# Optimization experiments

Hardware: AMD Instinct MI355X
Metric: run time of the kernel (lower is better)

Reference implementation:

```python
import jax, jax.numpy as jnp
import numpy as np
from jax import lax

N, D, M, H = 8192, 32, 8, 128
ATOL = 1e-5
RTOL = 1e-5
MAX_STEPS = 10   # bounded adaptive dopri5 iterations (accept/reject with masking)
DT0 = 0.25


def setup_inputs() -> dict:
    key = jax.random.key(0)
    ks = jax.random.split(key, 6)
    p = lambda k, shape, s: jax.random.normal(k, shape, jnp.float32) * s
    return {
        "z": jax.random.normal(ks[0], (N, D), jnp.float32),
        "G_w": p(ks[1], (M, D), 0.3),
        "W1": p(ks[2], (H, D), (1.0 / D) ** 0.5),
        "b1": jnp.zeros((H,), jnp.float32),
        "W2": p(ks[3], (H, H), (1.0 / H) ** 0.5),
        "b2": jnp.zeros((H,), jnp.float32),
        "W3": p(ks[4], (D, H), (1.0 / H) ** 0.5),
        "b3": jnp.zeros((D,), jnp.float32),
        "T": jnp.ones((1,), jnp.float32),
    }


def qpnf_forward(z, G_w, W1, b1, W2, b2, W3, b3, T):
    d = z.shape[1]

    def mlp(x):  # dF network: d -> 128 -> 128 -> d
        h = jax.nn.relu(x @ W1.T + b1)
        h = jax.nn.relu(h @ W2.T + b2)
        return h @ W3.T + b3

    # G is linear (no bias) so jacrev(G)(x) == G_w for every sample; the batched
    # dG @ dG^T solves collapse to one shared (m,m) solve / (d,d) projector.
    A = G_w @ G_w.T                       # (m, m)
    AinvG = jnp.linalg.solve(A, G_w)      # (m, d) = A^{-1} W
    P = G_w.T @ AinvG                     # (d, d) null-space projector W^T A^{-1} W
    IP = jnp.eye(d, dtype=z.dtype) - P
    trP = jnp.trace(P)

    jac_mlp = jax.vmap(jax.jacrev(lambda xi: mlp(xi[None, :])[0]))  # (N,d,d)

    def f(y):  # augmented state y = [x | logp], dlogp/dt = -div(dx/dx)
        x = y[:, :d]
        dF = mlp(x)                        # (N, d)
        g = x @ G_w.T                      # (N, m)
        dz = -(dF @ IP) - g @ AinvG        # -(eta_J) - (eta_C)
        JdF = jac_mlp(x)                   # (N, d, d)
        # J_f = -(I-P) JdF - P  ->  dlogp = -trace(J_f)
        dlogp = jnp.einsum('jk,nkj->n', IP, JdF) + trP
        return jnp.concatenate([dz, dlogp[:, None]], axis=1)

    def rk_step(y, dt):  # Dormand-Prince 5(4)
        k1 = f(y)
        k2 = f(y + dt * (0.2 * k1))
        k3 = f(y + dt * (3/40 * k1 + 9/40 * k2))
        k4 = f(y + dt * (44/45 * k1 - 56/15 * k2 + 32/9 * k3))
        k5 = f(y + dt * (19372/6561 * k1 - 25360/2187 * k2 + 64448/6561 * k3 - 212/729 * k4))
        k6 = f(y + dt * (9017/3168 * k1 - 355/33 * k2 + 46732/5247 * k3 + 49/176 * k4 - 5103/18656 * k5))
        y1 = y + dt * (35/384 * k1 + 500/1113 * k3 + 125/192 * k4 - 2187/6784 * k5 + 11/84 * k6)
        k7 = f(y1)
        err = dt * ((35/384 - 5179/57600) * k1 + (500/1113 - 7571/16695) * k3
                    + (125/192 - 393/640) * k4 + (-2187/6784 + 92097/339200) * k5
                    + (11/84 - 187/2100) * k6 - (1/40) * k7)
        return y1, err

    t1 = 2.0 * T[0]  # eval path: integration_times[-1] *= 2
    y0 = jnp.concatenate([z, jnp.zeros((z.shape[0], 1), z.dtype)], axis=1)

    def body(carry, _):
        t, dt, y = carry
        done = t >= t1 - 1e-9
        dtc = jnp.where(done, jnp.asarray(1e-3, z.dtype), jnp.minimum(dt, t1 - t))
        y1, ev = rk_step(y, dtc)
        tol = ATOL + RTOL * jnp.maximum(jnp.abs(y), jnp.abs(y1))
        errn = jnp.sqrt(jnp.mean((ev / tol) ** 2))
        accept = jnp.logical_and(~done, errn <= 1.0)
        y_new = jnp.where(accept, y1, y)
        t_new = jnp.where(accept, t + dtc, t)
        factor = jnp.clip(0.9 * errn ** (-0.2), 0.2, 10.0)
        dt_new = jnp.where(done, dt, jnp.clip(dtc * factor, 1e-6, t1))
        dt_new = lax.stop_gradient(dt_new)
        return (t_new, dt_new, y_new), None

    init = (jnp.asarray(0.0, z.dtype), jnp.asarray(DT0, z.dtype), y0)
    (_, _, yT), _ = lax.scan(body, init, None, length=MAX_STEPS)
    return yT[:, :d]


def reference(z, G_w, W1, b1, W2, b2, W3, b3, T):
    return qpnf_forward(z, G_w, W1, b1, W2, b2, W3, b3, T)
```

## Files before the change

### kernel.cpp

```cpp
#include <hip/hip_runtime.h>
#include <hip/hip_cooperative_groups.h>
#include <math.h>

namespace cg = cooperative_groups;
typedef float4 f4;

#define NT 512
#define RB 32

#define WS_R     0
#define WS_W2T   16384
#define WS_PART  32768
#define WS_YZ    35328
#define WS_Y1Z   297472
#define WS_YL    559616
#define WS_Y1L   567808
#define WS_KZ    576000
#define WS_KL    2411008
#define WS_TOTAL 2468352

#define L_W1T   0
#define L_C3    4096
#define L_P     8192
#define L_HST   9216
#define L_XST   13824
#define L_B1    14976
#define L_B2    15104
#define L_C0    15232
#define L_GS    15264
#define L_AAUG  15520
#define L_AINVG 15648
#define L_MISC  15904
#define LDS_FLOATS 15905
#define L_RED   L_XST

__device__ const float ACO[5][5] = {
  { 0.2f, 0.f, 0.f, 0.f, 0.f },
  { (float)(3.0/40.0), (float)(9.0/40.0), 0.f, 0.f, 0.f },
  { (float)(44.0/45.0), (float)(-56.0/15.0), (float)(32.0/9.0), 0.f, 0.f },
  { (float)(19372.0/6561.0), (float)(-25360.0/2187.0), (float)(64448.0/6561.0), (float)(-212.0/729.0), 0.f },
  { (float)(9017.0/3168.0), (float)(-355.0/33.0), (float)(46732.0/5247.0), (float)(49.0/176.0), (float)(-5103.0/18656.0) }
};

#define B1C ((float)(35.0/384.0))
#define B3C ((float)(500.0/1113.0))
#define B4C ((float)(125.0/192.0))
#define B5C ((float)(-2187.0/6784.0))
#define B6C ((float)(11.0/84.0))

#define E1C ((float)(35.0/384.0 - 5179.0/57600.0))
#define E3C ((float)(500.0/1113.0 - 7571.0/16695.0))
#define E4C ((float)(125.0/192.0 - 393.0/640.0))
#define E5C ((float)(-2187.0/6784.0 + 92097.0/339200.0))
#define E6C ((float)(11.0/84.0 - 187.0/2100.0))
#define E7C ((float)(-1.0/40.0))

__device__ __forceinline__ f4 ld4(const float* p){ return *(const f4*)p; }
__device__ __forceinline__ void st4(float* p, f4 v){ *(f4*)p = v; }

__device__ void assemble_x(float* lds, const float* __restrict__ ws, int r0, int tid,
                           float dtc, const float* co, int np)
{
  __syncthreads();
  if (tid < 256){
    const int r = tid >> 3, jj = (tid & 7) * 4;
    const int base = (r0 + r) * 32 + jj;
    f4 y = ld4(&ws[WS_YZ + base]);
    float sx = 0.f, sy = 0.f, sz = 0.f, sw = 0.f;
    for (int p = 0; p < np; p++){
      f4 kv = ld4(&ws[WS_KZ + p * 262144 + base]);
      float c = co[p];
      sx += c * kv.x; sy += c * kv.y; sz += c * kv.z; sw += c * kv.w;
    }
    lds[L_XST + (jj + 0) * 36 + r] = y.x + dtc * sx;
    lds[L_XST + (jj + 1) * 36 + r] = y.y + dtc * sy;
    lds[L_XST + (jj + 2) * 36 + r] = y.z + dtc * sz;
    lds[L_XST + (jj + 3) * 36 + r] = y.w + dtc * sw;
  }
  __syncthreads();
}

__device__ void eval_f(float* lds, float* __restrict__ ws, int r0, int tid,
                       float trP, int kout)
{
  const int cg = tid & 31, kh = (tid >> 5) & 1, wv = tid >> 6;
  const int row4 = 4 * wv;

  float a1[4][4];
#pragma unroll
  for (int i = 0; i < 4; i++)
#pragma unroll
    for (int j = 0; j < 4; j++) a1[i][j] = 0.f;
#pragma unroll 4
  for (int t = 0; t < 16; t++){
    const int k = kh * 16 + t;
    f4 av = ld4(&lds[L_XST + k * 36 + row4]);
    f4 bv = ld4(&lds[L_W1T + k * 128 + 4 * cg]);
    const float* ap = (const float*)&av;
    const float* bp = (const float*)&bv;
#pragma unroll
    for (int i = 0; i < 4; i++)
#pragma unroll
      for (int j = 0; j < 4; j++) a1[i][j] += bp[i] * ap[j];
  }
#pragma unroll
  for (int i = 0; i < 4; i++)
#pragma unroll
    for (int j = 0; j < 4; j++) a1[i][j] += __shfl_xor(a1[i][j], 32);
  if (kh == 0){
    f4 b1v = ld4(&lds[L_B1 + 4 * cg]);
    const float* b1p = (const float*)&b1v;
#pragma unroll
    for (int i = 0; i < 4; i++){
      f4 hv; float* hp = (float*)&hv;
#pragma unroll
      for (int j = 0; j < 4; j++) hp[j] = fmaxf(a1[i][j] + b1p[i], 0.f);
      st4(&lds[L_HST + (4 * cg + i) * 36 + row4], hv);
    }
  }
  __syncthreads();

  float ah[4][4], at[4][4];
#pragma unroll
  for (int i = 0; i < 4; i++)
#pragma unroll
    for (int j = 0; j < 4; j++){ ah[i][j] = 0.f; at[i][j] = 0.f; }
  const f4* W2T4 = (const f4*)&ws[WS_W2T];
  const f4* R4   = (const f4*)&ws[WS_R];
  const int kb = kh * 64;
  f4 wb[4], rb[4];
#pragma unroll
  for (int u = 0; u < 4; u++){
    wb[u] = W2T4[(kb + u) * 32 + cg];
    rb[u] = R4[(kb + u) * 32 + cg];
  }
#pragma unroll 1
  for (int g = 0; g < 16; g++){
    f4 wc[4], rc[4];
#pragma unroll
    for (int u = 0; u < 4; u++){ wc[u] = wb[u]; rc[u] = rb[u]; }
    if (g < 15){
      const int kn = kb + (g + 1) * 4;
#pragma unroll
      for (int u = 0; u < 4; u++){
        wb[u] = W2T4[(kn + u) * 32 + cg];
        rb[u] = R4[(kn + u) * 32 + cg];
      }
    }
#pragma unroll
    for (int u = 0; u < 4; u++){
      const int k = kb + g * 4 + u;
      f4 av = ld4(&lds[L_HST + k * 36 + row4]);
      const float* ap = (const float*)&av;
      const float* wp = (const float*)&wc[u];
      const float* rp = (const float*)&rc[u];
      float m[4];
#pragma unroll
      for (int j = 0; j < 4; j++) m[j] = (ap[j] > 0.f) ? 1.f : 0.f;
#pragma unroll
      for (int i = 0; i < 4; i++)
#pragma unroll
        for (int j = 0; j < 4; j++){
          ah[i][j] += wp[i] * ap[j];
          at[i][j] += rp[i] * m[j];
        }
    }
  }
#pragma unroll
  for (int i = 0; i < 4; i++)
#pragma unroll
    for (int j = 0; j < 4; j++){
      ah[i][j] += __shfl_xor(ah[i][j], 32);
      at[i][j] += __shfl_xor(at[i][j], 32);
    }

  f4 b2v = ld4(&lds[L_B2 + 4 * cg]);
  const float* b2p = (const float*)&b2v;
  float h2v[4][4]; float dl[4] = {0.f, 0.f, 0.f, 0.f};
#pragma unroll
  for (int i = 0; i < 4; i++)
#pragma unroll
    for (int j = 0; j < 4; j++){
      float pre = ah[i][j] + b2p[i];
      float hv = fmaxf(pre, 0.f);
      h2v[i][j] = hv;
      if (pre > 0.f) dl[j] += at[i][j];
    }
#pragma unroll
  for (int mk = 1; mk < 32; mk <<= 1){
#pragma unroll
    for (int j = 0; j < 4; j++) dl[j] += __shfl_xor(dl[j], mk, 64);
  }
  __syncthreads();
  if (kh == 0){
#pragma unroll
    for (int i = 0; i < 4; i++){
      f4 hv; float* hp = (float*)&hv;
#pragma unroll
      for (int j = 0; j < 4; j++) hp[j] = h2v[i][j];
      st4(&lds[L_HST + (4 * cg + i) * 36 + row4], hv);
    }
    if (cg == 0){
#pragma unroll
      for (int j = 0; j < 4; j++)
        ws[WS_KL + kout * 8192 + r0 + row4 + j] = dl[j] + trP;
    }
  }
  __syncthreads();

  float a3[4] = {0.f, 0.f, 0.f, 0.f};
#pragma unroll 8
  for (int t = 0; t < 64; t++){
    const int b = kh * 64 + t;
    f4 av = ld4(&lds[L_HST + b * 36 + row4]);
    const float* ap = (const float*)&av;
    float w3 = lds[L_C3 + b * 32 + cg];
#pragma unroll
    for (int j = 0; j < 4; j++) a3[j] += ap[j] * w3;
  }
#pragma unroll 8
  for (int t = 0; t < 16; t++){
    const int q = kh * 16 + t;
    f4 av = ld4(&lds[L_XST + q * 36 + row4]);
    const float* ap = (const float*)&av;
    float pv = lds[L_P + q * 32 + cg];
#pragma unroll
    for (int j = 0; j < 4; j++) a3[j] += ap[j] * pv;
  }
#pragma unroll
  for (int j = 0; j < 4; j++) a3[j] += __shfl_xor(a3[j], 32);
  if (kh == 0){
    float c0v = lds[L_C0 + cg];
#pragma unroll
    for (int j = 0; j < 4; j++)
      ws[WS_KZ + kout * 262144 + (r0 + row4 + j) * 32 + cg] = -(a3[j] + c0v);
  }
}

__global__ void __launch_bounds__(NT, 2)
qpnf_kernel(const float* __restrict__ z, const float* __restrict__ Gw,
            const float* __restrict__ W1g, const float* __restrict__ b1g,
            const float* __restrict__ W2g, const float* __restrict__ b2g,
            const float* __restrict__ W3g, const float* __restrict__ b3g,
            const float* __restrict__ Tg, float* __restrict__ out,
            float* __restrict__ ws)
{
  __shared__ float lds[LDS_FLOATS];
  const int tid = threadIdx.x;
  const int bid = blockIdx.x;
  const int r0 = bid * RB;
  cg::grid_group grid = cg::this_grid();

  for (int i = 0; i < 8; i++){
    int idx = tid + i * NT;
    int h = idx >> 5, j = idx & 31;
    lds[L_W1T + j * 128 + h] = W1g[idx];
  }
  if (tid < 128){ lds[L_B1 + tid] = b1g[tid]; lds[L_B2 + tid] = b2g[tid]; }
  if (tid < 256) lds[L_GS + tid] = Gw[tid];
  __syncthreads();

  if (tid < 64){
    int i = tid >> 3, j = tid & 7;
    float s = 0.f;
    for (int k = 0; k < 32; k++) s += lds[L_GS + i * 32 + k] * lds[L_GS + j * 32 + k];
    lds[L_AAUG + i * 16 + j] = s;
    lds[L_AAUG + i * 16 + 8 + j] = (i == j) ? 1.f : 0.f;
  }
  __syncthreads();
  if (tid == 0){
    float* A = &lds[L_AAUG];
    for (int c = 0; c < 8; c++){
      int p = c; float mx = fabsf(A[c * 16 + c]);
      for (int r = c + 1; r < 8; r++){
        float v = fabsf(A[r * 16 + c]);
        if (v > mx){ mx = v; p = r; }
      }
      if (p != c)
        for (int q = 0; q < 16; q++){ float t = A[c*16+q]; A[c*16+q] = A[p*16+q]; A[p*16+q] = t; }
      float pv = 1.0f / A[c * 16 + c];
      for (int q = 0; q < 16; q++) A[c * 16 + q] *= pv;
      for (int r = 0; r < 8; r++) if (r != c){
        float fct = A[r * 16 + c];
        for (int q = 0; q < 16; q++) A[r * 16 + q] -= fct * A[c * 16 + q];
      }
    }
  }
  __syncthreads();
  if (tid < 256){
    int m = tid >> 5, d = tid & 31;
    float s = 0.f;
    for (int q = 0; q < 8; q++) s += lds[L_AAUG + m * 16 + 8 + q] * lds[L_GS + q * 32 + d];
    lds[L_AINVG + m * 32 + d] = s;
  }
  __syncthreads();
  for (int i4 = 0; i4 < 2; i4++){
    int idx = tid + i4 * NT;
    int i = idx >> 5, j = idx & 31;
    float s = 0.f;
    for (int m = 0; m < 8; m++) s += lds[L_GS + m * 32 + i] * lds[L_AINVG + m * 32 + j];
    lds[L_P + i * 32 + j] = s;
  }
  __syncthreads();
  float* IPl = &lds[L_XST];
  for (int i4 = 0; i4 < 2; i4++){
    int idx = tid + i4 * NT;
    int i = idx >> 5, j = idx & 31;
    IPl[i * 32 + j] = ((i == j) ? 1.f : 0.f) - lds[L_P + i * 32 + j];
  }
  if (tid == 0){
    float s = 0.f;
    for (int i = 0; i < 32; i++) s += lds[L_P + i * 32 + i];
    lds[L_MISC] = s;
  }
  __syncthreads();
  for (int i4 = 0; i4 < 8; i4++){
    int idx = tid + i4 * NT;
    int b = idx >> 5, c = idx & 31;
    float s = 0.f;
    for (int i = 0; i < 32; i++) s += W3g[i * 128 + b] * IPl[i * 32 + c];
    lds[L_C3 + b * 32 + c] = s;
  }
  if (tid < 32){
    float s = 0.f;
    for (int i = 0; i < 32; i++) s += b3g[i] * IPl[i * 32 + tid];
    lds[L_C0 + tid] = s;
  }
  for (int i4 = 0; i4 < 8; i4++){
    int idx = tid + i4 * NT;
    int j = idx >> 7, b = idx & 127;
    float s = 0.f;
    for (int k = 0; k < 32; k++) s += IPl[j * 32 + k] * W3g[k * 128 + b];
    lds[L_HST + j * 128 + b] = s;
  }
  __syncthreads();
  if (bid < 128 && tid < 128){
    int a = bid;
    float s = 0.f;
    for (int j = 0; j < 32; j++) s += W1g[a * 32 + j] * lds[L_HST + j * 128 + tid];
    ws[WS_R + a * 128 + tid] = s * W2g[tid * 128 + a];
  }
  if (bid >= 128 && tid < 128){
    int a = bid - 128;
    ws[WS_W2T + a * 128 + tid] = W2g[tid * 128 + a];
  }
  if (tid < 256){
    const int r = tid >> 3, jj = (tid & 7) * 4;
    const int base = (r0 + r) * 32 + jj;
    st4(&ws[WS_YZ + base], ld4(&z[base]));
  }
  if (tid < RB) ws[WS_YL + r0 + tid] = 0.f;

  const float trP = lds[L_MISC];
  const float t1 = 2.0f * Tg[0];

  grid.sync();

  float t_cur = 0.f, dt_cur = 0.25f;
  bool prev_acc = false;

  for (int step = 0; step < 10; step++){
    if (t_cur >= t1 - 1e-9f) break;
    const float dtc = fminf(dt_cur, t1 - t_cur);

    for (int s = 1; s <= 6; s++){
      if (s == 1 && step > 0){
        if (prev_acc){
          if (tid < 256){
            const int r = tid >> 3, jj = (tid & 7) * 4;
            const int base = (r0 + r) * 32 + jj;
            st4(&ws[WS_KZ + 0 * 262144 + base], ld4(&ws[WS_KZ + 6 * 262144 + base]));
          }
          if (tid < RB) ws[WS_KL + 0 * 8192 + r0 + tid] = ws[WS_KL + 6 * 8192 + r0 + tid];
        }
        continue;
      }
      assemble_x(lds, ws, r0, tid, dtc, ACO[s >= 2 ? s - 2 : 0], s - 1);
      eval_f(lds, ws, r0, tid, trP, s - 1);
    }

    __syncthreads();
    if (tid < 256){
      const int r = tid >> 3, jj = (tid & 7) * 4;
      const int base = (r0 + r) * 32 + jj;
      f4 y   = ld4(&ws[WS_YZ + base]);
      f4 k1v = ld4(&ws[WS_KZ + 0 * 262144 + base]);
      f4 k3v = ld4(&ws[WS_KZ + 2 * 262144 + base]);
      f4 k4v = ld4(&ws[WS_KZ + 3 * 262144 + base]);
      f4 k5v = ld4(&ws[WS_KZ + 4 * 262144 + base]);
      f4 k6v = ld4(&ws[WS_KZ + 5 * 262144 + base]);
      f4 x;
      x.x = y.x + dtc * (B1C*k1v.x + B3C*k3v.x + B4C*k4v.x + B5C*k5v.x + B6C*k6v.x);
      x.y = y.y + dtc * (B1C*k1v.y + B3C*k3v.y + B4C*k4v.y + B5C*k5v.y + B6C*k6v.y);
      x.z = y.z + dtc * (B1C*k1v.z + B3C*k3v.z + B4C*k4v.z + B5C*k5v.z + B6C*k6v.z);
      x.w = y.w + dtc * (B1C*k1v.w + B3C*k3v.w + B4C*k4v.w + B5C*k5v.w + B6C*k6v.w);
      st4(&ws[WS_Y1Z + base], x);
      lds[L_XST + (jj + 0) * 36 + r] = x.x;
      lds[L_XST + (jj + 1) * 36 + r] = x.y;
      lds[L_XST + (jj + 2) * 36 + r] = x.z;
      lds[L_XST + (jj + 3) * 36 + r] = x.w;
    }
    if (tid < RB){
      int n = r0 + tid;
      float s = B1C * ws[WS_KL + 0*8192 + n] + B3C * ws[WS_KL + 2*8192 + n]
              + B4C * ws[WS_KL + 3*8192 + n] + B5C * ws[WS_KL + 4*8192 + n]
              + B6C * ws[WS_KL + 5*8192 + n];
      ws[WS_Y1L + n] = ws[WS_YL + n] + dtc * s;
    }
    __syncthreads();
    eval_f(lds, ws, r0, tid, trP, 6);
    __syncthreads();

    float sacc = 0.f;
    if (tid < 256){
      const int r = tid >> 3, jj = (tid & 7) * 4;
      const int base = (r0 + r) * 32 + jj;
      f4 k1v = ld4(&ws[WS_KZ + 0 * 262144 + base]);
      f4 k3v = ld4(&ws[WS_KZ + 2 * 262144 + base]);
      f4 k4v = ld4(&ws[WS_KZ + 3 * 262144 + base]);
      f4 k5v = ld4(&ws[WS_KZ + 4 * 262144 + base]);
      f4 k6v = ld4(&ws[WS_KZ + 5 * 262144 + base]);
      f4 k7v = ld4(&ws[WS_KZ + 6 * 262144 + base]);
      f4 yv  = ld4(&ws[WS_YZ + base]);
      f4 y1v = ld4(&ws[WS_Y1Z + base]);
      float ev, tol, q;
      ev = dtc * (E1C*k1v.x + E3C*k3v.x + E4C*k4v.x + E5C*k5v.x + E6C*k6v.x + E7C*k7v.x);
      tol = 1e-5f + 1e-5f * fmaxf(fabsf(yv.x), fabsf(y1v.x)); q = ev / tol; sacc += q * q;
      ev = dtc * (E1C*k1v.y + E3C*k3v.y + E4C*k4v.y + E5C*k5v.y + E6C*k6v.y + E7C*k7v.y);
      tol = 1e-5f + 1e-5f * fmaxf(fabsf(yv.y), fabsf(y1v.y)); q = ev / tol; sacc += q * q;
      ev = dtc * (E1C*k1v.z + E3C*k3v.z + E4C*k4v.z + E5C*k5v.z + E6C*k6v.z + E7C*k7v.z);
      tol = 1e-5f + 1e-5f * fmaxf(fabsf(yv.z), fabsf(y1v.z)); q = ev / tol; sacc += q * q;
      ev = dtc * (E1C*k1v.w + E3C*k3v.w + E4C*k4v.w + E5C*k5v.w + E6C*k6v.w + E7C*k7v.w);
      tol = 1e-5f + 1e-5f * fmaxf(fabsf(yv.w), fabsf(y1v.w)); q = ev / tol; sacc += q * q;
    }
    if (tid < RB){
      int n = r0 + tid;
      float evl = dtc * (E1C * ws[WS_KL + 0*8192 + n] + E3C * ws[WS_KL + 2*8192 + n]
                + E4C * ws[WS_KL + 3*8192 + n] + E5C * ws[WS_KL + 4*8192 + n]
                + E6C * ws[WS_KL + 5*8192 + n] + E7C * ws[WS_KL + 6*8192 + n]);
      float toll = 1e-5f + 1e-5f * fmaxf(fabsf(ws[WS_YL + n]), fabsf(ws[WS_Y1L + n]));
      float ql = evl / toll; sacc += ql * ql;
    }
    lds[L_RED + tid] = sacc; __syncthreads();
    for (int o = 256; o > 0; o >>= 1){
      if (tid < o) lds[L_RED + tid] += lds[L_RED + tid + o];
      __syncthreads();
    }
    if (tid == 0) ws[WS_PART + step * 256 + bid] = lds[L_RED + 0];

    grid.sync();

    if (tid < 256) lds[L_RED + tid] = ws[WS_PART + step * 256 + tid];
    __syncthreads();
    for (int o = 128; o > 0; o >>= 1){
      if (tid < o) lds[L_RED + tid] += lds[L_RED + tid + o];
      __syncthreads();
    }
    const float errn = sqrtf(lds[L_RED + 0] / 270336.0f);
    __syncthreads();

    const bool accept = (errn <= 1.0f);
    if (accept){
      if (tid < 256){
        const int r = tid >> 3, jj = (tid & 7) * 4;
        const int base = (r0 + r) * 32 + jj;
        st4(&ws[WS_YZ + base], ld4(&ws[WS_Y1Z + base]));
      }
      if (tid < RB) ws[WS_YL + r0 + tid] = ws[WS_Y1L + r0 + tid];
      t_cur += dtc;
    }
    float fac = 0.9f * powf(errn, -0.2f);
    fac = fminf(fmaxf(fac, 0.2f), 10.0f);
    dt_cur = fminf(fmaxf(dtc * fac, 1e-6f), t1);
    prev_acc = accept;
  }

  if (tid < 256){
    const int r = tid >> 3, jj = (tid & 7) * 4;
    const int base = (r0 + r) * 32 + jj;
    st4(&out[base], ld4(&ws[WS_YZ + base]));
  }
}

extern "C" void kernel_launch(void* const* d_in, const int* in_sizes, int n_in,
                              void* d_out, int out_size, void* d_ws, size_t ws_size,
                              hipStream_t stream)
{
  (void)in_sizes; (void)n_in; (void)out_size;
  const float* z  = (const float*)d_in[0];
  const float* Gw = (const float*)d_in[1];
  const float* W1 = (const float*)d_in[2];
  const float* b1 = (const float*)d_in[3];
  const float* W2 = (const float*)d_in[4];
  const float* b2 = (const float*)d_in[5];
  const float* W3 = (const float*)d_in[6];
  const float* b3 = (const float*)d_in[7];
  const float* T  = (const float*)d_in[8];
  float* out = (float*)d_out;
  float* ws  = (float*)d_ws;
  if (ws_size < (size_t)WS_TOTAL * sizeof(float)) return;

  void* args[] = { (void*)&z, (void*)&Gw, (void*)&W1, (void*)&b1, (void*)&W2,
                   (void*)&b2, (void*)&W3, (void*)&b3, (void*)&T, (void*)&out,
                   (void*)&ws };
  hipLaunchCooperativeKernel((const void*)qpnf_kernel, dim3(256), dim3(NT),
                             args, 0, stream);
}
```

Baseline: 1.336 ms.

## Split layer-2 matmul and Jacobian-trace work across two 512-thread groups

The block doubles from 512 to 1024 threads. One half computes the W2 forward product and the output layer, and the other half computes the R-weighted ReLU-mask product used for the divergence term. This halves the per-thread register accumulators and doubles the waves available to hide latency. The cost is idle threads in the layer-1 stage, extra LDS traffic because the mask is re-read from shared memory, and a larger block that may limit occupancy or the cooperative-launch residency. The L_RED reduction buffer must now hold 1024 entries, and it is unclear whether it was sized for that.

Result: slower. 1.644 ms (+23.1%).

```diff
diff --git a/kernel.cpp b/kernel.cpp
--- a/kernel.cpp
+++ b/kernel.cpp
@@ -5,7 +5,7 @@
 namespace cg = cooperative_groups;
 typedef float4 f4;
 
-#define NT 512
+#define NT 1024
 #define RB 32
 
 #define WS_R     0
@@ -83,161 +83,185 @@
 __device__ void eval_f(float* lds, float* __restrict__ ws, int r0, int tid,
                        float trP, int kout)
 {
-  const int cg = tid & 31, kh = (tid >> 5) & 1, wv = tid >> 6;
+  const int cg = tid & 31, kh = (tid >> 5) & 1, wv = (tid >> 6) & 7, grp = tid >> 9;
   const int row4 = 4 * wv;
 
-  float a1[4][4];
+  if (grp == 0){
+    float a1[4][4];
+#pragma unroll
+    for (int i = 0; i < 4; i++)
+#pragma unroll
+      for (int j = 0; j < 4; j++) a1[i][j] = 0.f;
+#pragma unroll 4
+    for (int t = 0; t < 16; t++){
+      const int k = kh * 16 + t;
+      f4 av = ld4(&lds[L_XST + k * 36 + row4]);
+      f4 bv = ld4(&lds[L_W1T + k * 128 + 4 * cg]);
+      const float* ap = (const float*)&av;
+      const float* bp = (const float*)&bv;
+#pragma unroll
+      for (int i = 0; i < 4; i++)
+#pragma unroll
+        for (int j = 0; j < 4; j++) a1[i][j] += bp[i] * ap[j];
+    }
+#pragma unroll
+    for (int i = 0; i < 4; i++)
+#pragma unroll
+      for (int j = 0; j < 4; j++) a1[i][j] += __shfl_xor(a1[i][j], 32);
+    if (kh == 0){
+      f4 b1v = ld4(&lds[L_B1 + 4 * cg]);
+      const float* b1p = (const float*)&b1v;
+#pragma unroll
+      for (int i = 0; i < 4; i++){
+        f4 hv; float* hp = (float*)&hv;
+#pragma unroll
+        for (int j = 0; j < 4; j++) hp[j] = fmaxf(a1[i][j] + b1p[i], 0.f);
+        st4(&lds[L_HST + (4 * cg + i) * 36 + row4], hv);
+      }
+    }
+  }
+  __syncthreads();
+
+  const int kb = kh * 64;
+  float ac[4][4];
 #pragma unroll
   for (int i = 0; i < 4; i++)
 #pragma unroll
-    for (int j = 0; j < 4; j++) a1[i][j] = 0.f;
-#pragma unroll 4
-  for (int t = 0; t < 16; t++){
-    const int k = kh * 16 + t;
-    f4 av = ld4(&lds[L_XST + k * 36 + row4]);
-    f4 bv = ld4(&lds[L_W1T + k * 128 + 4 * cg]);
-    const float* ap = (const float*)&av;
-    const float* bp = (const float*)&bv;
+    for (int j = 0; j < 4; j++) ac[i][j] = 0.f;
+
+  const f4* M4 = (const f4*)&ws[(grp == 0) ? WS_W2T : WS_R];
+  f4 mb[4];
+#pragma unroll
+  for (int u = 0; u < 4; u++) mb[u] = M4[(kb + u) * 32 + cg];
+
+  if (grp == 0){
+#pragma unroll 1
+    for (int g = 0; g < 16; g++){
+      f4 mc[4];
+#pragma unroll
+      for (int u = 0; u < 4; u++) mc[u] = mb[u];
+      if (g < 15){
+        const int kn = kb + (g + 1) * 4;
+#pragma unroll
+        for (int u = 0; u < 4; u++) mb[u] = M4[(kn + u) * 32 + cg];
+      }
+#pragma unroll
+      for (int u = 0; u < 4; u++){
+        const int k = kb + g * 4 + u;
+        f4 av = ld4(&lds[L_HST + k * 36 + row4]);
+        const float* ap = (const float*)&av;
+        const float* wp = (const float*)&mc[u];
+#pragma unroll
+        for (int i = 0; i < 4; i++)
+#pragma unroll
+          for (int j = 0; j < 4; j++) ac[i][j] += wp[i] * ap[j];
+      }
+    }
+  } else {
+#pragma unroll 1
+    for (int g = 0; g < 16; g++){
+      f4 mc[4];
+#pragma unroll
+      for (int u = 0; u < 4; u++) mc[u] = mb[u];
+      if (g < 15){
+        const int kn = kb + (g + 1) * 4;
+#pragma unroll
+        for (int u = 0; u < 4; u++) mb[u] = M4[(kn + u) * 32 + cg];
+      }
+#pragma unroll
+      for (int u = 0; u < 4; u++){
+        const int k = kb + g * 4 + u;
+        f4 av = ld4(&lds[L_HST + k * 36 + row4]);
+        const float* ap = (const float*)&av;
+        const float* rp = (const float*)&mc[u];
+        float m[4];
+#pragma unroll
+        for (int j = 0; j < 4; j++) m[j] = (ap[j] > 0.f) ? 1.f : 0.f;
+#pragma unroll
+        for (int i = 0; i < 4; i++)
+#pragma unroll
+          for (int j = 0; j < 4; j++) ac[i][j] += rp[i] * m[j];
+      }
+    }
+  }
+#pragma unroll
+  for (int i = 0; i < 4; i++)
+#pragma unroll
+    for (int j = 0; j < 4; j++) ac[i][j] += __shfl_xor(ac[i][j], 32);
+
+  float h2v[4][4];
+  if (grp == 0){
+    f4 b2v = ld4(&lds[L_B2 + 4 * cg]);
+    const float* b2p = (const float*)&b2v;
 #pragma unroll
     for (int i = 0; i < 4; i++)
 #pragma unroll
-      for (int j = 0; j < 4; j++) a1[i][j] += bp[i] * ap[j];
-  }
-#pragma unroll
-  for (int i = 0; i < 4; i++)
-#pragma unroll
-    for (int j = 0; j < 4; j++) a1[i][j] += __shfl_xor(a1[i][j], 32);
-  if (kh == 0){
-    f4 b1v = ld4(&lds[L_B1 + 4 * cg]);
-    const float* b1p = (const float*)&b1v;
+      for (int j = 0; j < 4; j++) h2v[i][j] = fmaxf(ac[i][j] + b2p[i], 0.f);
+  }
+  __syncthreads();
+  if (grp == 0 && kh == 0){
 #pragma unroll
     for (int i = 0; i < 4; i++){
       f4 hv; float* hp = (float*)&hv;
 #pragma unroll
-      for (int j = 0; j < 4; j++) hp[j] = fmaxf(a1[i][j] + b1p[i], 0.f);
-      st4(&lds[L_HST + (4 * cg + i) * 36 + row4], hv);
-    }
-  }
-  __syncthreads();
-
-  float ah[4][4], at[4][4];
-#pragma unroll
-  for (int i = 0; i < 4; i++)
-#pragma unroll
-    for (int j = 0; j < 4; j++){ ah[i][j] = 0.f; at[i][j] = 0.f; }
-  const f4* W2T4 = (const f4*)&ws[WS_W2T];
-  const f4* R4   = (const f4*)&ws[WS_R];
-  const int kb = kh * 64;
-  f4 wb[4], rb[4];
-#pragma unroll
-  for (int u = 0; u < 4; u++){
-    wb[u] = W2T4[(kb + u) * 32 + cg];
-    rb[u] = R4[(kb + u) * 32 + cg];
-  }
-#pragma unroll 1
-  for (int g = 0; g < 16; g++){
-    f4 wc[4], rc[4];
-#pragma unroll
-    for (int u = 0; u < 4; u++){ wc[u] = wb[u]; rc[u] = rb[u]; }
-    if (g < 15){
-      const int kn = kb + (g + 1) * 4;
-#pragma unroll
-      for (int u = 0; u < 4; u++){
-        wb[u] = W2T4[(kn + u) * 32 + cg];
-        rb[u] = R4[(kn + u) * 32 + cg];
-      }
-    }
-#pragma unroll
-    for (int u = 0; u < 4; u++){
-      const int k = kb + g * 4 + u;
-      f4 av = ld4(&lds[L_HST + k * 36 + row4]);
-      const float* ap = (const float*)&av;
-      const float* wp = (const float*)&wc[u];
-      const float* rp = (const float*)&rc[u];
-      float m[4];
-#pragma unroll
-      for (int j = 0; j < 4; j++) m[j] = (ap[j] > 0.f) ? 1.f : 0.f;
-#pragma unroll
-      for (int i = 0; i < 4; i++)
-#pragma unroll
-        for (int j = 0; j < 4; j++){
-          ah[i][j] += wp[i] * ap[j];
-          at[i][j] += rp[i] * m[j];
-        }
-    }
-  }
-#pragma unroll
-  for (int i = 0; i < 4; i++)
-#pragma unroll
-    for (int j = 0; j < 4; j++){
-      ah[i][j] += __shfl_xor(ah[i][j], 32);
-      at[i][j] += __shfl_xor(at[i][j], 32);
-    }
-
-  f4 b2v = ld4(&lds[L_B2 + 4 * cg]);
-  const float* b2p = (const float*)&b2v;
-  float h2v[4][4]; float dl[4] = {0.f, 0.f, 0.f, 0.f};
-#pragma unroll
-  for (int i = 0; i < 4; i++)
-#pragma unroll
-    for (int j = 0; j < 4; j++){
-      float pre = ah[i][j] + b2p[i];
-      float hv = fmaxf(pre, 0.f);
-      h2v[i][j] = hv;
-      if (pre > 0.f) dl[j] += at[i][j];
-    }
-#pragma unroll
-  for (int mk = 1; mk < 32; mk <<= 1){
-#pragma unroll
-    for (int j = 0; j < 4; j++) dl[j] += __shfl_xor(dl[j], mk, 64);
-  }
-  __syncthreads();
-  if (kh == 0){
-#pragma unroll
-    for (int i = 0; i < 4; i++){
-      f4 hv; float* hp = (float*)&hv;
-#pragma unroll
       for (int j = 0; j < 4; j++) hp[j] = h2v[i][j];
       st4(&lds[L_HST + (4 * cg + i) * 36 + row4], hv);
     }
-    if (cg == 0){
+  }
+  __syncthreads();
+
+  if (grp == 1){
+    float dl[4] = {0.f, 0.f, 0.f, 0.f};
+#pragma unroll
+    for (int i = 0; i < 4; i++){
+      f4 hv = ld4(&lds[L_HST + (4 * cg + i) * 36 + row4]);
+      const float* hp = (const float*)&hv;
+#pragma unroll
+      for (int j = 0; j < 4; j++)
+        if (hp[j] > 0.f) dl[j] += ac[i][j];
+    }
+#pragma unroll
+    for (int mk = 1; mk < 32; mk <<= 1){
+#pragma unroll
+      for (int j = 0; j < 4; j++) dl[j] += __shfl_xor(dl[j], mk, 64);
+    }
+    if (kh == 0 && cg == 0){
 #pragma unroll
       for (int j = 0; j < 4; j++)
         ws[WS_KL + kout * 8192 + r0 + row4 + j] = dl[j] + trP;
     }
-  }
-  __syncthreads();
-
-  float a3[4] = {0.f, 0.f, 0.f, 0.f};
+  } else {
+    float a3[4] = {0.f, 0.f, 0.f, 0.f};
 #pragma unroll 8
-  for (int t = 0; t < 64; t++){
-    const int b = kh * 64 + t;
-    f4 av = ld4(&lds[L_HST + b * 36 + row4]);
-    const float* ap = (const float*)&av;
-    float w3 = lds[L_C3 + b * 32 + cg];
-#pragma unroll
-    for (int j = 0; j < 4; j++) a3[j] += ap[j] * w3;
-  }
+    for (int t = 0; t < 64; t++){
+      const int b = kh * 64 + t;
+      f4 av = ld4(&lds[L_HST + b * 36 + row4]);
+      const float* ap = (const float*)&av;
+      float w3 = lds[L_C3 + b * 32 + cg];
+#pragma unroll
+      for (int j = 0; j < 4; j++) a3[j] += ap[j] * w3;
+    }
 #pragma unroll 8
-  for (int t = 0; t < 16; t++){
-    const int q = kh * 16 + t;
-    f4 av = ld4(&lds[L_XST + q * 36 + row4]);
-    const float* ap = (const float*)&av;
-    float pv = lds[L_P + q * 32 + cg];
-#pragma unroll
-    for (int j = 0; j < 4; j++) a3[j] += ap[j] * pv;
-  }
-#pragma unroll
-  for (int j = 0; j < 4; j++) a3[j] += __shfl_xor(a3[j], 32);
-  if (kh == 0){
-    float c0v = lds[L_C0 + cg];
-#pragma unroll
-    for (int j = 0; j < 4; j++)
-      ws[WS_KZ + kout * 262144 + (r0 + row4 + j) * 32 + cg] = -(a3[j] + c0v);
+    for (int t = 0; t < 16; t++){
+      const int q = kh * 16 + t;
+      f4 av = ld4(&lds[L_XST + q * 36 + row4]);
+      const float* ap = (const float*)&av;
+      float pv = lds[L_P + q * 32 + cg];
+#pragma unroll
+      for (int j = 0; j < 4; j++) a3[j] += ap[j] * pv;
+    }
+#pragma unroll
+    for (int j = 0; j < 4; j++) a3[j] += __shfl_xor(a3[j], 32);
+    if (kh == 0){
+      float c0v = lds[L_C0 + cg];
+#pragma unroll
+      for (int j = 0; j < 4; j++)
+        ws[WS_KZ + kout * 262144 + (r0 + row4 + j) * 32 + cg] = -(a3[j] + c0v);
+    }
   }
 }
 
-__global__ void __launch_bounds__(NT, 2)
+__global__ void __launch_bounds__(NT, 4)
 qpnf_kernel(const float* __restrict__ z, const float* __restrict__ Gw,
             const float* __restrict__ W1g, const float* __restrict__ b1g,
             const float* __restrict__ W2g, const float* __restrict__ b2g,
@@ -251,7 +275,7 @@
   const int r0 = bid * RB;
   cg::grid_group grid = cg::this_grid();
 
-  for (int i = 0; i < 8; i++){
+  for (int i = 0; i < 4; i++){
     int idx = tid + i * NT;
     int h = idx >> 5, j = idx & 31;
     lds[L_W1T + j * 128 + h] = W1g[idx];
@@ -294,18 +318,16 @@
     lds[L_AINVG + m * 32 + d] = s;
   }
   __syncthreads();
-  for (int i4 = 0; i4 < 2; i4++){
-    int idx = tid + i4 * NT;
-    int i = idx >> 5, j = idx & 31;
+  {
+    int i = tid >> 5, j = tid & 31;
     float s = 0.f;
     for (int m = 0; m < 8; m++) s += lds[L_GS + m * 32 + i] * lds[L_AINVG + m * 32 + j];
     lds[L_P + i * 32 + j] = s;
   }
   __syncthreads();
   float* IPl = &lds[L_XST];
-  for (int i4 = 0; i4 < 2; i4++){
-    int idx = tid + i4 * NT;
-    int i = idx >> 5, j = idx & 31;
+  {
+    int i = tid >> 5, j = tid & 31;
     IPl[i * 32 + j] = ((i == j) ? 1.f : 0.f) - lds[L_P + i * 32 + j];
   }
   if (tid == 0){
@@ -314,7 +336,7 @@
     lds[L_MISC] = s;
   }
   __syncthreads();
-  for (int i4 = 0; i4 < 8; i4++){
+  for (int i4 = 0; i4 < 4; i4++){
     int idx = tid + i4 * NT;
     int b = idx >> 5, c = idx & 31;
     float s = 0.f;
@@ -326,7 +348,7 @@
     for (int i = 0; i < 32; i++) s += b3g[i] * IPl[i * 32 + tid];
     lds[L_C0 + tid] = s;
   }
-  for (int i4 = 0; i4 < 8; i4++){
+  for (int i4 = 0; i4 < 4; i4++){
     int idx = tid + i4 * NT;
     int j = idx >> 7, b = idx & 127;
     float s = 0.f;
@@ -442,7 +464,7 @@
       float ql = evl / toll; sacc += ql * ql;
     }
     lds[L_RED + tid] = sacc; __syncthreads();
-    for (int o = 256; o > 0; o >>= 1){
+    for (int o = 512; o > 0; o >>= 1){
       if (tid < o) lds[L_RED + tid] += lds[L_RED + tid + o];
       __syncthreads();
     }
```

## Interleave W2T/R weights, transpose C3/P in LDS, double-buffer hidden tile

Applied to the files above, without the earlier changes.

Interleaves the W2 transpose and R matrices row by row in one workspace array, so each k-row's two float4 loads fall in the same region. Stores C3 and P transposed in LDS with padded strides, which lets the layer-3 and projector loops read four weights per float4 load instead of one scalar at a time. Writes the second hidden activation into a separate LDS buffer, which removes one __syncthreads between the layer-2 epilogue and the store. The cost is more LDS per block (about 21.8K floats instead of 15.9K), which could reduce occupancy under launch_bounds(512,2).

New measurement: 1.360 ms. About the same (+1.8%).

```diff
diff --git a/kernel.cpp b/kernel.cpp
--- a/kernel.cpp
+++ b/kernel.cpp
@@ -8,8 +8,7 @@
 #define NT 512
 #define RB 32
 
-#define WS_R     0
-#define WS_W2T   16384
+#define WS_WR    0
 #define WS_PART  32768
 #define WS_YZ    35328
 #define WS_Y1Z   297472
@@ -20,18 +19,20 @@
 #define WS_TOTAL 2468352
 
 #define L_W1T   0
-#define L_C3    4096
-#define L_P     8192
-#define L_HST   9216
-#define L_XST   13824
-#define L_B1    14976
-#define L_B2    15104
-#define L_C0    15232
-#define L_GS    15264
-#define L_AAUG  15520
-#define L_AINVG 15648
-#define L_MISC  15904
-#define LDS_FLOATS 15905
+#define L_C3T   4096
+#define L_P     8320
+#define L_PT    9344
+#define L_HST   10496
+#define L_HS2   15104
+#define L_XST   19712
+#define L_B1    20864
+#define L_B2    20992
+#define L_C0    21120
+#define L_GS    21152
+#define L_AAUG  21408
+#define L_AINVG 21536
+#define L_MISC  21792
+#define LDS_FLOATS 21793
 #define L_RED   L_XST
 
 __device__ const float ACO[5][5] = {
@@ -125,14 +126,13 @@
   for (int i = 0; i < 4; i++)
 #pragma unroll
     for (int j = 0; j < 4; j++){ ah[i][j] = 0.f; at[i][j] = 0.f; }
-  const f4* W2T4 = (const f4*)&ws[WS_W2T];
-  const f4* R4   = (const f4*)&ws[WS_R];
+  const f4* WR4 = (const f4*)&ws[WS_WR];
   const int kb = kh * 64;
   f4 wb[4], rb[4];
 #pragma unroll
   for (int u = 0; u < 4; u++){
-    wb[u] = W2T4[(kb + u) * 32 + cg];
-    rb[u] = R4[(kb + u) * 32 + cg];
+    wb[u] = WR4[(kb + u) * 64 + cg];
+    rb[u] = WR4[(kb + u) * 64 + 32 + cg];
   }
 #pragma unroll 1
   for (int g = 0; g < 16; g++){
@@ -143,8 +143,8 @@
       const int kn = kb + (g + 1) * 4;
 #pragma unroll
       for (int u = 0; u < 4; u++){
-        wb[u] = W2T4[(kn + u) * 32 + cg];
-        rb[u] = R4[(kn + u) * 32 + cg];
+        wb[u] = WR4[(kn + u) * 64 + cg];
+        rb[u] = WR4[(kn + u) * 64 + 32 + cg];
       }
     }
 #pragma unroll
@@ -191,14 +191,13 @@
 #pragma unroll
     for (int j = 0; j < 4; j++) dl[j] += __shfl_xor(dl[j], mk, 64);
   }
-  __syncthreads();
   if (kh == 0){
 #pragma unroll
     for (int i = 0; i < 4; i++){
       f4 hv; float* hp = (float*)&hv;
 #pragma unroll
       for (int j = 0; j < 4; j++) hp[j] = h2v[i][j];
-      st4(&lds[L_HST + (4 * cg + i) * 36 + row4], hv);
+      st4(&lds[L_HS2 + (4 * cg + i) * 36 + row4], hv);
     }
     if (cg == 0){
 #pragma unroll
@@ -209,23 +208,31 @@
   __syncthreads();
 
   float a3[4] = {0.f, 0.f, 0.f, 0.f};
-#pragma unroll 8
-  for (int t = 0; t < 64; t++){
-    const int b = kh * 64 + t;
-    f4 av = ld4(&lds[L_HST + b * 36 + row4]);
-    const float* ap = (const float*)&av;
-    float w3 = lds[L_C3 + b * 32 + cg];
-#pragma unroll
-    for (int j = 0; j < 4; j++) a3[j] += ap[j] * w3;
-  }
-#pragma unroll 8
+  const int bb = kh * 64;
+#pragma unroll 4
   for (int t = 0; t < 16; t++){
-    const int q = kh * 16 + t;
-    f4 av = ld4(&lds[L_XST + q * 36 + row4]);
-    const float* ap = (const float*)&av;
-    float pv = lds[L_P + q * 32 + cg];
-#pragma unroll
-    for (int j = 0; j < 4; j++) a3[j] += ap[j] * pv;
+    f4 cv = ld4(&lds[L_C3T + cg * 132 + bb + 4 * t]);
+    const float* cp = (const float*)&cv;
+#pragma unroll
+    for (int u = 0; u < 4; u++){
+      f4 av = ld4(&lds[L_HS2 + (bb + 4 * t + u) * 36 + row4]);
+      const float* ap = (const float*)&av;
+#pragma unroll
+      for (int j = 0; j < 4; j++) a3[j] += ap[j] * cp[u];
+    }
+  }
+  const int qq = kh * 16;
+#pragma unroll
+  for (int t = 0; t < 4; t++){
+    f4 pv = ld4(&lds[L_PT + cg * 36 + qq + 4 * t]);
+    const float* pp = (const float*)&pv;
+#pragma unroll
+    for (int u = 0; u < 4; u++){
+      f4 av = ld4(&lds[L_XST + (qq + 4 * t + u) * 36 + row4]);
+      const float* ap = (const float*)&av;
+#pragma unroll
+      for (int j = 0; j < 4; j++) a3[j] += ap[j] * pp[u];
+    }
   }
 #pragma unroll
   for (int j = 0; j < 4; j++) a3[j] += __shfl_xor(a3[j], 32);
@@ -316,10 +323,15 @@
   __syncthreads();
   for (int i4 = 0; i4 < 8; i4++){
     int idx = tid + i4 * NT;
-    int b = idx >> 5, c = idx & 31;
+    int b = idx & 127, c = idx >> 7;
     float s = 0.f;
     for (int i = 0; i < 32; i++) s += W3g[i * 128 + b] * IPl[i * 32 + c];
-    lds[L_C3 + b * 32 + c] = s;
+    lds[L_C3T + c * 132 + b] = s;
+  }
+  for (int i4 = 0; i4 < 2; i4++){
+    int idx = tid + i4 * NT;
+    int c = idx >> 5, q = idx & 31;
+    lds[L_PT + c * 36 + q] = lds[L_P + q * 32 + c];
   }
   if (tid < 32){
     float s = 0.f;
@@ -338,11 +350,11 @@
     int a = bid;
     float s = 0.f;
     for (int j = 0; j < 32; j++) s += W1g[a * 32 + j] * lds[L_HST + j * 128 + tid];
-    ws[WS_R + a * 128 + tid] = s * W2g[tid * 128 + a];
+    ws[WS_WR + a * 256 + 128 + tid] = s * W2g[tid * 128 + a];
   }
   if (bid >= 128 && tid < 128){
     int a = bid - 128;
-    ws[WS_W2T + a * 128 + tid] = W2g[tid * 128 + a];
+    ws[WS_WR + a * 256 + tid] = W2g[tid * 128 + a];
   }
   if (tid < 256){
     const int r = tid >> 3, jj = (tid & 7) * 4;
```
